# Kernel tuning notes

Measured on AMD Instinct MI355X. Metric: run time of the kernel, lower is better.

The kernel has to match this reference:

```python
import jax, jax.numpy as jnp
import numpy as np

IN_DIM = 768
N_HEADS = 12
HEAD_DIM = IN_DIM // N_HEADS


def setup_inputs() -> dict:
    key = jax.random.key(0)
    k1, k2, k3, k4, k5 = jax.random.split(key, 5)
    x = jax.random.normal(k1, (2, 2048, IN_DIM), dtype=jnp.float32)
    s = 1.0 / np.sqrt(IN_DIM)
    W_qkv = jax.random.uniform(k2, (IN_DIM, 3 * IN_DIM), jnp.float32, -s, s)
    b_qkv = jax.random.uniform(k3, (3 * IN_DIM,), jnp.float32, -s, s)
    W_out = jax.random.uniform(k4, (IN_DIM, IN_DIM), jnp.float32, -s, s)
    b_out = jax.random.uniform(k5, (IN_DIM,), jnp.float32, -s, s)
    return {"x": x, "W_qkv": W_qkv, "b_qkv": b_qkv, "W_out": W_out, "b_out": b_out}


def reference(x, W_qkv, b_qkv, W_out, b_out):
    B, N, D = x.shape
    qkv = x @ W_qkv + b_qkv  # [B, N, 3D]
    qkv = qkv.reshape(B, N, 3, N_HEADS, HEAD_DIM)
    qkv = jnp.transpose(qkv, (2, 0, 3, 1, 4))  # [3, B, H, N, Dh]
    q, k, v = qkv[0], qkv[1], qkv[2]
    scale = 1.0 / np.sqrt(HEAD_DIM)
    scores = jnp.einsum("bhqd,bhkd->bhqk", q, k) * scale  # [B, H, N, N]
    attn = jax.nn.softmax(scores, axis=-1)
    out = jnp.einsum("bhqk,bhkd->bhqd", attn, v)  # [B, H, N, Dh]
    out = jnp.transpose(out, (0, 2, 1, 3)).reshape(B, N, D)
    return out @ W_out + b_out
```

## Files before the change

### kernel.cpp

```cpp
#include <hip/hip_runtime.h>

#define DEVI __device__ __forceinline__

typedef __attribute__((ext_vector_type(8))) short short8;
typedef __attribute__((ext_vector_type(4))) float f32x4;
typedef __attribute__((ext_vector_type(16))) float f32x16;

DEVI unsigned short f32_to_bf16(float f) {
  unsigned int u = __float_as_uint(f);
  u += 0x7fffu + ((u >> 16) & 1u);
  return (unsigned short)(u >> 16);
}
DEVI float bf16_to_f32(unsigned short h) {
  return __uint_as_float(((unsigned int)h) << 16);
}

DEVI void gld_lds16(const void* g, void* l) {
  __builtin_amdgcn_global_load_lds(
      (__attribute__((address_space(1))) void*)(g),
      (__attribute__((address_space(3))) void*)(l), 16, 0, 0);
}

__global__ __launch_bounds__(256) void k_prep(const float* __restrict__ x,
                                              const float* __restrict__ Wq,
                                              const float* __restrict__ Wo,
                                              unsigned short* __restrict__ Xb,
                                              unsigned short* __restrict__ Wq_t,
                                              unsigned short* __restrict__ Wo_t) {
  int blk = blockIdx.x;
  int tid = threadIdx.x;
  if (blk < 1536) {
    int i = blk * 256 + tid;
    const float* src = x + (size_t)i * 8;
    short8 v;
#pragma unroll
    for (int j = 0; j < 8; ++j) v[j] = (short)f32_to_bf16(src[j]);
    *(short8*)&Xb[(size_t)i * 8] = v;
    return;
  }
  const float* W;
  unsigned short* Wt;
  int kt, nt, K, N;
  if (blk < 3264) {
    int idx = blk - 1536;
    kt = idx % 24;
    nt = idx / 24;
    W = Wq;
    Wt = Wq_t;
    K = 768;
    N = 2304;
  } else {
    int idx = blk - 3264;
    kt = idx % 24;
    nt = idx / 24;
    W = Wo;
    Wt = Wo_t;
    K = 768;
    N = 768;
  }
  __shared__ float t[32][33];
#pragma unroll
  for (int p = 0; p < 4; ++p) {
    int idx = tid + p * 256;
    int rr = idx >> 5, cc = idx & 31;
    t[rr][cc] = W[(size_t)(kt * 32 + rr) * N + nt * 32 + cc];
  }
  __syncthreads();
#pragma unroll
  for (int p = 0; p < 4; ++p) {
    int idx = tid + p * 256;
    int rn = idx >> 5, ck = idx & 31;
    Wt[(size_t)(nt * 32 + rn) * K + kt * 32 + ck] = f32_to_bf16(t[ck][rn]);
  }
}

__global__ __launch_bounds__(256) void k_gemm_qkv(const unsigned short* __restrict__ A,
                                                  const unsigned short* __restrict__ Bt,
                                                  const float* __restrict__ bias,
                                                  int M, int N, int K,
                                                  unsigned short* __restrict__ Qo,
                                                  unsigned short* __restrict__ Ko,
                                                  unsigned short* __restrict__ Vo) {
  __shared__ __align__(16) unsigned short As[128 * 32];
  __shared__ __align__(16) unsigned short Bs[128 * 32];
  int tid = threadIdx.x;
  int tm = blockIdx.x, tn = blockIdx.y;
  int lane = tid & 63, wid = tid >> 6;
  int wr = wid >> 1, wc = wid & 1;
  int g = lane >> 4, lr = lane & 15;
  f32x4 acc[4][4] = {};
  int srow = tid >> 2;
  int scol = (tid & 3) * 8;
  const unsigned short* Ab = A + (size_t)tm * 128 * K;
  const unsigned short* Bb = Bt + (size_t)tn * 128 * K;
  for (int k0 = 0; k0 < K; k0 += 32) {
    gld_lds16(Ab + (size_t)srow * K + k0 + scol, &As[srow * 32 + scol]);
    gld_lds16(Ab + (size_t)(srow + 64) * K + k0 + scol, &As[(srow + 64) * 32 + scol]);
    gld_lds16(Bb + (size_t)srow * K + k0 + scol, &Bs[srow * 32 + scol]);
    gld_lds16(Bb + (size_t)(srow + 64) * K + k0 + scol, &Bs[(srow + 64) * 32 + scol]);
    __syncthreads();
    short8 a[4], b[4];
#pragma unroll
    for (int m = 0; m < 4; ++m)
      a[m] = *(const short8*)&As[(wr * 64 + m * 16 + lr) * 32 + g * 8];
#pragma unroll
    for (int n = 0; n < 4; ++n)
      b[n] = *(const short8*)&Bs[(wc * 64 + n * 16 + lr) * 32 + g * 8];
#pragma unroll
    for (int m = 0; m < 4; ++m)
#pragma unroll
      for (int n = 0; n < 4; ++n)
        acc[m][n] = __builtin_amdgcn_mfma_f32_16x16x32_bf16(a[m], b[n], acc[m][n], 0, 0, 0);
    __syncthreads();
  }
  const float QSCALE = 0.125f * 1.4426950408889634f;
#pragma unroll
  for (int m = 0; m < 4; ++m) {
#pragma unroll
    for (int n = 0; n < 4; ++n) {
      int col = tn * 128 + wc * 64 + n * 16 + lr;
      float bv = bias[col];
      int sec = (col >= 1536) ? 2 : ((col >= 768) ? 1 : 0);
      int c = col - sec * 768;
      int hh = c >> 6, d = c & 63;
#pragma unroll
      for (int j = 0; j < 4; ++j) {
        int row = tm * 128 + wr * 64 + m * 16 + g * 4 + j;
        int bb = row >> 11, nn = row & 2047;
        size_t dst = (((size_t)(bb * 12 + hh) << 11) + nn) * 64 + d;
        float outv = acc[m][n][j] + bv;
        if (sec == 0) {
          Qo[dst] = f32_to_bf16(outv * QSCALE);
        } else if (sec == 1) {
          Ko[dst] = f32_to_bf16(outv);
        } else {
          Vo[dst] = f32_to_bf16(outv);
        }
      }
    }
  }
}

__global__ __launch_bounds__(256) void k_gemm2(const unsigned short* __restrict__ A,
                                               const unsigned short* __restrict__ Bt,
                                               const float* __restrict__ bias,
                                               float* __restrict__ C,
                                               int M, int N, int K) {
  __shared__ __align__(16) unsigned short As[64 * 32];
  __shared__ __align__(16) unsigned short Bs[64 * 32];
  int tid = threadIdx.x;
  int tm = blockIdx.x, tn = blockIdx.y;
  int lane = tid & 63, wid = tid >> 6;
  int wr = wid >> 1, wc = wid & 1;
  int g = lane >> 4, lr = lane & 15;
  f32x4 acc[2][2] = {};
  int srow = tid >> 2;
  int scol = (tid & 3) * 8;
  const unsigned short* Ab = A + (size_t)tm * 64 * K;
  const unsigned short* Bb = Bt + (size_t)tn * 64 * K;
  for (int k0 = 0; k0 < K; k0 += 32) {
    gld_lds16(Ab + (size_t)srow * K + k0 + scol, &As[srow * 32 + scol]);
    gld_lds16(Bb + (size_t)srow * K + k0 + scol, &Bs[srow * 32 + scol]);
    __syncthreads();
    short8 a[2], b[2];
#pragma unroll
    for (int m = 0; m < 2; ++m)
      a[m] = *(const short8*)&As[(wr * 32 + m * 16 + lr) * 32 + g * 8];
#pragma unroll
    for (int n = 0; n < 2; ++n)
      b[n] = *(const short8*)&Bs[(wc * 32 + n * 16 + lr) * 32 + g * 8];
#pragma unroll
    for (int m = 0; m < 2; ++m)
#pragma unroll
      for (int n = 0; n < 2; ++n)
        acc[m][n] = __builtin_amdgcn_mfma_f32_16x16x32_bf16(a[m], b[n], acc[m][n], 0, 0, 0);
    __syncthreads();
  }
#pragma unroll
  for (int m = 0; m < 2; ++m) {
#pragma unroll
    for (int n = 0; n < 2; ++n) {
      int col = tn * 64 + wc * 32 + n * 16 + lr;
      float bv = bias[col];
#pragma unroll
      for (int j = 0; j < 4; ++j) {
        int row = tm * 64 + wr * 32 + m * 16 + g * 4 + j;
        C[(size_t)row * N + col] = acc[m][n][j] + bv;
      }
    }
  }
}

__global__ __launch_bounds__(256) void k_v_transpose(const unsigned short* __restrict__ Vc,
                                                     unsigned short* __restrict__ Vt) {
  int bh = blockIdx.x;
  int nt = blockIdx.y;
  __shared__ unsigned short s[64][65];
  int tid = threadIdx.x;
  int r = tid >> 2;
#pragma unroll
  for (int p = 0; p < 2; ++p) {
    int c = (tid & 3) + p * 4;
    short8 v = *(const short8*)&Vc[((size_t)(bh * 2048 + nt * 64 + r)) * 64 + c * 8];
#pragma unroll
    for (int ii = 0; ii < 8; ++ii) s[r][c * 8 + ii] = (unsigned short)v[ii];
  }
  __syncthreads();
  int d = tid >> 2;
#pragma unroll
  for (int p = 0; p < 2; ++p) {
    int c = (tid & 3) + p * 4;
    short8 w;
#pragma unroll
    for (int ii = 0; ii < 8; ++ii) w[ii] = (short)s[c * 8 + ii][d];
    *(short8*)&Vt[((size_t)bh * 64 + d) * 2048 + nt * 64 + c * 8] = w;
  }
}


#define ATTN_STAGE(KSB, VSB, T)                                                          \
  {                                                                                      \
    int kv0 = (T) * 64;                                                                  \
    _Pragma("unroll") for (int it = 0; it < 2; ++it) {                                   \
      int L = tid + it * 256;                                                            \
      int rw = L >> 3, s7 = L & 7;                                                       \
      gld_lds16(Kb + (size_t)(khead + kv0 + rw) * 64 + ((s7 ^ (rw & 7)) * 8),            \
                &KSB[L * 8]);                                                            \
      gld_lds16(Vt + (size_t)(vhead + rw) * 2048 + kv0 + ((s7 ^ (rw & 7)) * 8),          \
                &VSB[L * 8]);                                                            \
    }                                                                                    \
  }

#define BUILD_PA(S)                                                                      \
  {                                                                                      \
    unsigned int b0, a0, e0, c0;                                                         \
    asm("v_cvt_pk_bf16_f32 %0, %1, %2" : "=v"(b0) : "v"(S[0]), "v"(S[1]));               \
    asm("v_cvt_pk_bf16_f32 %0, %1, %2" : "=v"(a0) : "v"(S[4]), "v"(S[5]));               \
    asm("v_permlane32_swap_b32 %0, %1" : "+v"(b0), "+v"(a0));                            \
    asm("v_cvt_pk_bf16_f32 %0, %1, %2" : "=v"(e0) : "v"(S[2]), "v"(S[3]));               \
    asm("v_cvt_pk_bf16_f32 %0, %1, %2" : "=v"(c0) : "v"(S[6]), "v"(S[7]));               \
    asm("v_permlane32_swap_b32 %0, %1" : "+v"(e0), "+v"(c0));                            \
    paw[0][0] = b0; paw[0][1] = e0; paw[0][2] = a0; paw[0][3] = c0;                      \
    unsigned int b1, a1, e1, c1;                                                         \
    asm("v_cvt_pk_bf16_f32 %0, %1, %2" : "=v"(b1) : "v"(S[8]), "v"(S[9]));               \
    asm("v_cvt_pk_bf16_f32 %0, %1, %2" : "=v"(a1) : "v"(S[12]), "v"(S[13]));             \
    asm("v_permlane32_swap_b32 %0, %1" : "+v"(b1), "+v"(a1));                            \
    asm("v_cvt_pk_bf16_f32 %0, %1, %2" : "=v"(e1) : "v"(S[10]), "v"(S[11]));             \
    asm("v_cvt_pk_bf16_f32 %0, %1, %2" : "=v"(c1) : "v"(S[14]), "v"(S[15]));             \
    asm("v_permlane32_swap_b32 %0, %1" : "+v"(e1), "+v"(c1));                            \
    paw[1][0] = b1; paw[1][1] = e1; paw[1][2] = a1; paw[1][3] = c1;                      \
  }

#define PROC_TILE(KSB, VSB)                                                              \
  {                                                                                      \
    f32x16 sa = {};                                                                      \
    __builtin_amdgcn_s_setprio(1);                                                       \
    _Pragma("unroll") for (int ds = 0; ds < 4; ++ds) {                                   \
      short8 kf = *(const short8*)&KSB[(kh * 32 + ln31) * 64 + (((ds * 2 + hi) ^ ln7) * 8)]; \
      sa = __builtin_amdgcn_mfma_f32_32x32x16_bf16(kf, qf[ds], sa, 0, 0, 0);             \
    }                                                                                    \
    __builtin_amdgcn_s_setprio(0);                                                       \
    _Pragma("unroll") for (int i = 0; i < 16; ++i) {                                     \
      float pv = exp2f(sa[i]);                                                           \
      sa[i] = pv;                                                                        \
      lrun += pv;                                                                        \
    }                                                                                    \
    unsigned int paw[2][4];                                                              \
    BUILD_PA(sa)                                                                         \
    __builtin_amdgcn_s_setprio(1);                                                       \
    _Pragma("unroll") for (int kl = 0; kl < 2; ++kl) {                                   \
      union {                                                                            \
        unsigned int u[4];                                                               \
        short8 s8;                                                                       \
      } pu;                                                                              \
      pu.u[0] = paw[kl][0];                                                              \
      pu.u[1] = paw[kl][1];                                                              \
      pu.u[2] = paw[kl][2];                                                              \
      pu.u[3] = paw[kl][3];                                                              \
      int ksg = kh * 2 + kl;                                                             \
      short8 vb0 = *(const short8*)&VSB[ln31 * 64 + (((ksg * 2 + hi) ^ ln7) * 8)];       \
      short8 vb1 = *(const short8*)&VSB[(32 + ln31) * 64 + (((ksg * 2 + hi) ^ ln7) * 8)]; \
      oacc0 = __builtin_amdgcn_mfma_f32_32x32x16_bf16(pu.s8, vb0, oacc0, 0, 0, 0);       \
      oacc1 = __builtin_amdgcn_mfma_f32_32x32x16_bf16(pu.s8, vb1, oacc1, 0, 0, 0);       \
    }                                                                                    \
    __builtin_amdgcn_s_setprio(0);                                                       \
  }

__global__ __launch_bounds__(256, 4) void k_attn(const unsigned short* __restrict__ Qb,
                                                 const unsigned short* __restrict__ Kb,
                                                 const unsigned short* __restrict__ Vt,
                                                 unsigned short* __restrict__ Xh) {
  int bh = blockIdx.x;
  int qb = blockIdx.y;
  int b = bh / 12, h = bh - b * 12;
  __shared__ __align__(16) unsigned short LDSbuf[4 * 64 * 64];
  unsigned short* Ks0 = LDSbuf;
  unsigned short* Vs0 = LDSbuf + 64 * 64;
  unsigned short* Ks1 = LDSbuf + 2 * 64 * 64;
  unsigned short* Vs1 = LDSbuf + 3 * 64 * 64;
  int tid = threadIdx.x;
  int wid = tid >> 6, lane = tid & 63;
  int qh = wid >> 1, kh = wid & 1;
  int ln31 = lane & 31, hi = lane >> 5, ln7 = lane & 7;
  int khead = bh * 2048;
  int vhead = bh * 64;
  int q0 = qb * 64 + qh * 32;

  short8 qf[4];
#pragma unroll
  for (int ds = 0; ds < 4; ++ds)
    qf[ds] = *(const short8*)&Qb[(size_t)(khead + q0 + ln31) * 64 + ds * 16 + hi * 8];

  float lrun = 0.f;
  f32x16 oacc0 = {}, oacc1 = {};

  ATTN_STAGE(Ks0, Vs0, 0);
  __syncthreads();
#pragma unroll 1
  for (int tt = 0; tt < 16; ++tt) {
    ATTN_STAGE(Ks1, Vs1, 2 * tt + 1);
    PROC_TILE(Ks0, Vs0);
    __syncthreads();
    if (tt < 15) ATTN_STAGE(Ks0, Vs0, 2 * tt + 2);
    PROC_TILE(Ks1, Vs1);
    __syncthreads();
  }

  lrun += __shfl_xor(lrun, 32, 64);

  float* scr = (float*)LDSbuf;
  if (kh == 1) {
    float* p = scr + (size_t)(qh * 64 + lane) * 33;
#pragma unroll
    for (int i = 0; i < 16; ++i) {
      p[i] = oacc0[i];
      p[16 + i] = oacc1[i];
    }
    p[32] = lrun;
  }
  __syncthreads();
  if (kh == 0) {
    float* p = scr + (size_t)(qh * 64 + lane) * 33;
#pragma unroll
    for (int i = 0; i < 16; ++i) {
      oacc0[i] += p[i];
      oacc1[i] += p[16 + i];
    }
    lrun += p[32];
    float linv = 1.0f / lrun;
#pragma unroll
    for (int r = 0; r < 16; ++r) {
      int qrow = (r & 3) + 8 * (r >> 2) + 4 * hi;
      float lf = __shfl(linv, qrow, 64);
      int grow = b * 2048 + q0 + qrow;
      int colb = h * 64 + ln31;
      Xh[(size_t)grow * 768 + colb] = f32_to_bf16(oacc0[r] * lf);
      Xh[(size_t)grow * 768 + colb + 32] = f32_to_bf16(oacc1[r] * lf);
    }
  }
}

extern "C" void kernel_launch(void* const* d_in, const int* in_sizes, int n_in,
                              void* d_out, int out_size, void* d_ws, size_t ws_size,
                              hipStream_t stream) {
  const float* x = (const float*)d_in[0];
  const float* W_qkv = (const float*)d_in[1];
  const float* b_qkv = (const float*)d_in[2];
  const float* W_out = (const float*)d_in[3];
  const float* b_out = (const float*)d_in[4];
  float* out = (float*)d_out;
  char* ws = (char*)d_ws;

  unsigned short* Xh = (unsigned short*)(ws + 0);
  unsigned short* Xb = (unsigned short*)(ws + 18874368);
  unsigned short* Wq_t = (unsigned short*)(ws + 25165824);
  unsigned short* Wo_t = (unsigned short*)(ws + 28704768);
  unsigned short* Qb = (unsigned short*)(ws + 32243712);
  unsigned short* Kb = (unsigned short*)(ws + 38535168);
  unsigned short* Vc = (unsigned short*)(ws + 44826624);
  unsigned short* Vt = (unsigned short*)(ws + 51118080);

  k_prep<<<3840, 256, 0, stream>>>(x, W_qkv, W_out, Xb, Wq_t, Wo_t);
  k_gemm_qkv<<<dim3(32, 18), 256, 0, stream>>>(Xb, Wq_t, b_qkv, 4096, 2304, 768, Qb, Kb, Vc);
  k_v_transpose<<<dim3(24, 32), 256, 0, stream>>>(Vc, Vt);
  k_attn<<<dim3(24, 32), 256, 0, stream>>>(Qb, Kb, Vt, Xh);
  k_gemm2<<<dim3(64, 12), 256, 0, stream>>>(Xh, Wo_t, b_out, out, 4096, 768, 768);
}
```

Measured before the change: 100.9 us.

## Fuse V transpose into QKV GEMM epilogue and shrink N-tile to 64

The QKV projection now writes V straight into the transposed [bh, d, n] layout from its epilogue, which removes the separate transpose kernel and its round trip through global memory. To make this simple, the GEMM tile becomes 128x64 so each block covers a single Q/K/V section and head, and the section is computed once per block. Each wave now owns 32 rows across all 64 columns, and the grid doubles to 32x36. The smaller tile lowers data reuse per block, and the V stores are 8-byte writes strided by 2048 elements.

New measurement: 95.57 us. -5.3%, faster.

```diff
diff --git a/kernel.cpp b/kernel.cpp
--- a/kernel.cpp
+++ b/kernel.cpp
@@ -3,6 +3,7 @@
 #define DEVI __device__ __forceinline__
 
 typedef __attribute__((ext_vector_type(8))) short short8;
+typedef __attribute__((ext_vector_type(4))) short s16x4;
 typedef __attribute__((ext_vector_type(4))) float f32x4;
 typedef __attribute__((ext_vector_type(16))) float f32x16;
 
@@ -80,61 +81,62 @@
                                                   int M, int N, int K,
                                                   unsigned short* __restrict__ Qo,
                                                   unsigned short* __restrict__ Ko,
-                                                  unsigned short* __restrict__ Vo) {
+                                                  unsigned short* __restrict__ Vt) {
   __shared__ __align__(16) unsigned short As[128 * 32];
-  __shared__ __align__(16) unsigned short Bs[128 * 32];
+  __shared__ __align__(16) unsigned short Bs[64 * 32];
   int tid = threadIdx.x;
   int tm = blockIdx.x, tn = blockIdx.y;
   int lane = tid & 63, wid = tid >> 6;
-  int wr = wid >> 1, wc = wid & 1;
   int g = lane >> 4, lr = lane & 15;
-  f32x4 acc[4][4] = {};
+  f32x4 acc[2][4] = {};
   int srow = tid >> 2;
   int scol = (tid & 3) * 8;
   const unsigned short* Ab = A + (size_t)tm * 128 * K;
-  const unsigned short* Bb = Bt + (size_t)tn * 128 * K;
+  const unsigned short* Bb = Bt + (size_t)tn * 64 * K;
   for (int k0 = 0; k0 < K; k0 += 32) {
     gld_lds16(Ab + (size_t)srow * K + k0 + scol, &As[srow * 32 + scol]);
     gld_lds16(Ab + (size_t)(srow + 64) * K + k0 + scol, &As[(srow + 64) * 32 + scol]);
     gld_lds16(Bb + (size_t)srow * K + k0 + scol, &Bs[srow * 32 + scol]);
-    gld_lds16(Bb + (size_t)(srow + 64) * K + k0 + scol, &Bs[(srow + 64) * 32 + scol]);
-    __syncthreads();
-    short8 a[4], b[4];
-#pragma unroll
-    for (int m = 0; m < 4; ++m)
-      a[m] = *(const short8*)&As[(wr * 64 + m * 16 + lr) * 32 + g * 8];
+    __syncthreads();
+    short8 a[2], b[4];
+#pragma unroll
+    for (int m = 0; m < 2; ++m)
+      a[m] = *(const short8*)&As[(wid * 32 + m * 16 + lr) * 32 + g * 8];
 #pragma unroll
     for (int n = 0; n < 4; ++n)
-      b[n] = *(const short8*)&Bs[(wc * 64 + n * 16 + lr) * 32 + g * 8];
-#pragma unroll
-    for (int m = 0; m < 4; ++m)
+      b[n] = *(const short8*)&Bs[(n * 16 + lr) * 32 + g * 8];
+#pragma unroll
+    for (int m = 0; m < 2; ++m)
 #pragma unroll
       for (int n = 0; n < 4; ++n)
         acc[m][n] = __builtin_amdgcn_mfma_f32_16x16x32_bf16(a[m], b[n], acc[m][n], 0, 0, 0);
     __syncthreads();
   }
   const float QSCALE = 0.125f * 1.4426950408889634f;
-#pragma unroll
-  for (int m = 0; m < 4; ++m) {
+  int sec = tn / 12;
+  int cb = tn * 64 - sec * 768;
+#pragma unroll
+  for (int m = 0; m < 2; ++m) {
 #pragma unroll
     for (int n = 0; n < 4; ++n) {
-      int col = tn * 128 + wc * 64 + n * 16 + lr;
-      float bv = bias[col];
-      int sec = (col >= 1536) ? 2 : ((col >= 768) ? 1 : 0);
-      int c = col - sec * 768;
+      int c = cb + n * 16 + lr;
       int hh = c >> 6, d = c & 63;
-#pragma unroll
-      for (int j = 0; j < 4; ++j) {
-        int row = tm * 128 + wr * 64 + m * 16 + g * 4 + j;
-        int bb = row >> 11, nn = row & 2047;
-        size_t dst = (((size_t)(bb * 12 + hh) << 11) + nn) * 64 + d;
-        float outv = acc[m][n][j] + bv;
-        if (sec == 0) {
-          Qo[dst] = f32_to_bf16(outv * QSCALE);
-        } else if (sec == 1) {
-          Ko[dst] = f32_to_bf16(outv);
-        } else {
-          Vo[dst] = f32_to_bf16(outv);
+      float bv = bias[tn * 64 + n * 16 + lr];
+      int rowb = tm * 128 + wid * 32 + m * 16 + g * 4;
+      int bb = rowb >> 11, nn = rowb & 2047;
+      int bh = bb * 12 + hh;
+      if (sec == 2) {
+        s16x4 v4;
+#pragma unroll
+        for (int j = 0; j < 4; ++j) v4[j] = (short)f32_to_bf16(acc[m][n][j] + bv);
+        *(s16x4*)&Vt[((size_t)bh * 64 + d) * 2048 + nn] = v4;
+      } else {
+        unsigned short* dst0 = (sec == 0) ? Qo : Ko;
+        float sc = (sec == 0) ? QSCALE : 1.0f;
+#pragma unroll
+        for (int j = 0; j < 4; ++j) {
+          size_t dst = (((size_t)bh << 11) + nn + j) * 64 + d;
+          dst0[dst] = f32_to_bf16((acc[m][n][j] + bv) * sc);
         }
       }
     }
@@ -191,32 +193,6 @@
   }
 }
 
-__global__ __launch_bounds__(256) void k_v_transpose(const unsigned short* __restrict__ Vc,
-                                                     unsigned short* __restrict__ Vt) {
-  int bh = blockIdx.x;
-  int nt = blockIdx.y;
-  __shared__ unsigned short s[64][65];
-  int tid = threadIdx.x;
-  int r = tid >> 2;
-#pragma unroll
-  for (int p = 0; p < 2; ++p) {
-    int c = (tid & 3) + p * 4;
-    short8 v = *(const short8*)&Vc[((size_t)(bh * 2048 + nt * 64 + r)) * 64 + c * 8];
-#pragma unroll
-    for (int ii = 0; ii < 8; ++ii) s[r][c * 8 + ii] = (unsigned short)v[ii];
-  }
-  __syncthreads();
-  int d = tid >> 2;
-#pragma unroll
-  for (int p = 0; p < 2; ++p) {
-    int c = (tid & 3) + p * 4;
-    short8 w;
-#pragma unroll
-    for (int ii = 0; ii < 8; ++ii) w[ii] = (short)s[c * 8 + ii][d];
-    *(short8*)&Vt[((size_t)bh * 64 + d) * 2048 + nt * 64 + c * 8] = w;
-  }
-}
-
 
 #define ATTN_STAGE(KSB, VSB, T)                                                          \
   {                                                                                      \
@@ -271,7 +247,7 @@
     _Pragma("unroll") for (int kl = 0; kl < 2; ++kl) {                                   \
       union {                                                                            \
         unsigned int u[4];                                                               \
-        short8 s8;                                                                       \
+        short8 s8;                                                                      \
       } pu;                                                                              \
       pu.u[0] = paw[kl][0];                                                              \
       pu.u[1] = paw[kl][1];                                                              \
@@ -377,12 +353,10 @@
   unsigned short* Wo_t = (unsigned short*)(ws + 28704768);
   unsigned short* Qb = (unsigned short*)(ws + 32243712);
   unsigned short* Kb = (unsigned short*)(ws + 38535168);
-  unsigned short* Vc = (unsigned short*)(ws + 44826624);
   unsigned short* Vt = (unsigned short*)(ws + 51118080);
 
   k_prep<<<3840, 256, 0, stream>>>(x, W_qkv, W_out, Xb, Wq_t, Wo_t);
-  k_gemm_qkv<<<dim3(32, 18), 256, 0, stream>>>(Xb, Wq_t, b_qkv, 4096, 2304, 768, Qb, Kb, Vc);
-  k_v_transpose<<<dim3(24, 32), 256, 0, stream>>>(Vc, Vt);
+  k_gemm_qkv<<<dim3(32, 36), 256, 0, stream>>>(Xb, Wq_t, b_qkv, 4096, 2304, 768, Qb, Kb, Vt);
   k_attn<<<dim3(24, 32), 256, 0, stream>>>(Qb, Kb, Vt, Xh);
   k_gemm2<<<dim3(64, 12), 256, 0, stream>>>(Xh, Wo_t, b_out, out, 4096, 768, 768);
 }
```
